# Optimization experiments

Hardware: AMD Instinct MI355X
Metric: run time of the kernel (lower is better)

The kernel has to match this reference:

```python
import jax, jax.numpy as jnp
import numpy as np

D_MODEL = 512
D_INNER = 2 * D_MODEL      # 1024
DT_RANK = D_MODEL // 16    # 32
D_STATE = 16
D_CONV = 4
NB_LAYERS = 3
BATCH = 64
SEQ = 201
CITY = 200
EPS = 1e-5


def setup_inputs() -> dict:
    key = jax.random.key(0)
    ks = jax.random.split(key, 12)
    def rn(k, shape, scale=0.02):
        return jax.random.normal(k, shape, jnp.float32) * scale
    A_init = jnp.tile(jnp.arange(1, D_STATE + 1, dtype=jnp.float32)[None, None, :],
                      (NB_LAYERS, D_INNER, 1))
    return {
        "x": jax.random.uniform(ks[0], (BATCH, SEQ, 2), jnp.float32),
        "city_count": CITY,
        "embed_W": rn(ks[1], (D_MODEL, 2), 0.5),
        "embed_b": jnp.zeros((D_MODEL,), jnp.float32),
        "norm_w": jnp.ones((NB_LAYERS, D_MODEL), jnp.float32),
        "norm_b": jnp.zeros((NB_LAYERS, D_MODEL), jnp.float32),
        "in_W": rn(ks[2], (NB_LAYERS, 2 * D_INNER, D_MODEL)),
        "conv_w": rn(ks[3], (NB_LAYERS, D_INNER, D_CONV), 0.1),
        "conv_b": jnp.zeros((NB_LAYERS, D_INNER), jnp.float32),
        "xproj_W": rn(ks[4], (NB_LAYERS, DT_RANK + 2 * D_STATE, D_INNER)),
        "dtproj_W": rn(ks[5], (NB_LAYERS, D_INNER, DT_RANK), 0.1),
        "dtproj_b": rn(ks[6], (NB_LAYERS, D_INNER), 0.5),
        "A_log": jnp.log(A_init),
        "Dskip": jnp.ones((NB_LAYERS, D_INNER), jnp.float32),
        "out_W": rn(ks[7], (NB_LAYERS, D_MODEL, D_INNER)),
        "normf_w": jnp.ones((D_MODEL,), jnp.float32),
        "normf_b": jnp.zeros((D_MODEL,), jnp.float32),
        "head_W": rn(ks[8], (CITY, D_MODEL)),
    }


def _silu(v):
    return v * jax.nn.sigmoid(v)


def _layernorm(v, w, b):
    v = v.astype(jnp.float32)
    mu = v.mean(-1, keepdims=True)
    var = ((v - mu) ** 2).mean(-1, keepdims=True)
    return (v - mu) * jax.lax.rsqrt(var + EPS) * w + b


def _rmsnorm(v, w, b):
    v = v.astype(jnp.float32)
    ms = (v * v).mean(-1, keepdims=True)
    return v * jax.lax.rsqrt(ms + EPS) * w + b


def _mamba_mixer(h, in_W, cw, cb, xp_W, dt_W, dt_b, A_log, Dv, o_W):
    B, L, _ = h.shape
    xz = jnp.einsum('bld,ed->ble', h, in_W)              # (B,L,2*di)
    xc, z = jnp.split(xz, 2, axis=-1)
    # causal depthwise conv over time
    xt = xc.transpose(0, 2, 1)                           # (B,di,L)
    xt = jax.lax.conv_general_dilated(
        xt, cw[:, None, :], (1,), [(D_CONV - 1, 0)],
        dimension_numbers=('NCH', 'OIH', 'NCH'),
        feature_group_count=D_INNER)
    u = _silu((xt + cb[None, :, None]).transpose(0, 2, 1))   # (B,L,di)
    x_dbl = jnp.einsum('bld,ed->ble', u, xp_W)
    dt_r = x_dbl[..., :DT_RANK]
    Bm = x_dbl[..., DT_RANK:DT_RANK + D_STATE]
    Cm = x_dbl[..., DT_RANK + D_STATE:]
    dt = jax.nn.softplus(jnp.einsum('blr,dr->bld', dt_r, dt_W) + dt_b)
    A = -jnp.exp(A_log)                                  # (di,n)

    def step(hst, ins):
        dt_t, B_t, C_t, u_t = ins                        # (B,di),(B,n),(B,n),(B,di)
        dA = jnp.exp(dt_t[..., None] * A)                # (B,di,n)
        hst = dA * hst + (dt_t * u_t)[..., None] * B_t[:, None, :]
        y = jnp.einsum('bdn,bn->bd', hst, C_t)
        return hst, y

    h0 = jnp.zeros((B, D_INNER, D_STATE), h.dtype)
    _, ys = jax.lax.scan(step, h0, (dt.transpose(1, 0, 2), Bm.transpose(1, 0, 2),
                                    Cm.transpose(1, 0, 2), u.transpose(1, 0, 2)))
    y = ys.transpose(1, 0, 2) + Dv * u
    y = y * _silu(z)
    return jnp.einsum('bld,ed->ble', y, o_W)


def reference(x, city_count, embed_W, embed_b, norm_w, norm_b, in_W, conv_w, conv_b,
              xproj_W, dtproj_W, dtproj_b, A_log, Dskip, out_W, normf_w, normf_b, head_W):
    h = jnp.einsum('blc,dc->bld', x, embed_W) + embed_b
    residual = None
    for i in range(NB_LAYERS):
        residual = h if residual is None else h + residual   # residual in fp32
        hn = _layernorm(residual, norm_w[i], norm_b[i])
        h = _mamba_mixer(hn, in_W[i], conv_w[i], conv_b[i], xproj_W[i],
                         dtproj_W[i], dtproj_b[i], A_log[i], Dskip[i], out_W[i])
    residual = h + residual
    xf = _rmsnorm(residual, normf_w, normf_b)                # final fused RMSNorm
    logits = jnp.einsum('bld,cd->blc', xf, head_W)           # output head -> city logits
    return logits
```

## Files before the change

### kernel.cpp

```cpp
#include <hip/hip_runtime.h>
#include <hip/hip_fp16.h>
#include <math.h>

#define D_MODEL 512
#define D_INNER 1024
#define DT_RANK 32
#define D_STATE 16
#define D_CONV 4
#define NB_LAYERS 3
#define BATCH 64
#define SEQ 201
#define CITY 200
#define M_ROWS (BATCH * SEQ)
#define M_PAD 12928
#define EPS 1e-5f
#define NCH 8
#define CL 26

typedef __attribute__((ext_vector_type(8))) short short8;
typedef __attribute__((ext_vector_type(8))) unsigned short ushort8;
typedef __attribute__((ext_vector_type(4))) float f32x4;

__device__ __forceinline__ float sigmoidf_(float x) { return 1.f / (1.f + __expf(-x)); }

__device__ __forceinline__ unsigned short f2b(float f) {
  union { float f; unsigned int u; } v; v.f = f;
  unsigned int r = (v.u + 0x7fff + ((v.u >> 16) & 1)) >> 16;
  return (unsigned short)r;
}
__device__ __forceinline__ float b2f(unsigned short h) {
  union { unsigned int u; float f; } v; v.u = ((unsigned int)h) << 16; return v.f;
}
__device__ __forceinline__ unsigned short f2h(float f) {
  __half h = __float2half(f); return *(unsigned short*)&h;
}
__device__ __forceinline__ float h2f(unsigned short u) {
  __half h = *(__half*)&u; return __half2float(h);
}

__device__ __forceinline__ void gload_lds16(const void* g, void* l) {
  __builtin_amdgcn_global_load_lds(
      (const __attribute__((address_space(1))) void*)g,
      (__attribute__((address_space(3))) void*)l, 16, 0, 0);
}

__device__ __forceinline__ void exp_vec(float dtv, const float* __restrict__ Areg,
                                        bool fast, float* __restrict__ e) {
  if (fast) {
    float e1 = __expf(-dtv);
    e[0] = e1;
    e[1] = e1 * e1;
    e[2] = e[1] * e1;
    e[3] = e[1] * e[1];
    e[4] = e[3] * e1;
    e[5] = e[3] * e[1];
    e[6] = e[3] * e[2];
    e[7] = e[3] * e[3];
    e[8] = e[7] * e1;
    e[9] = e[7] * e[1];
    e[10] = e[7] * e[2];
    e[11] = e[7] * e[3];
    e[12] = e[7] * e[4];
    e[13] = e[7] * e[5];
    e[14] = e[7] * e[6];
    e[15] = e[7] * e[7];
  } else {
#pragma unroll
    for (int n = 0; n < D_STATE; ++n) e[n] = __expf(dtv * Areg[n]);
  }
}
__device__ __forceinline__ bool a_is_arange(const float* __restrict__ Areg) {
  bool f = true;
#pragma unroll
  for (int n = 0; n < D_STATE; ++n)
    f = f && (fabsf(Areg[n] + (float)(n + 1)) < 1e-4f * (float)(n + 1));
  return f;
}

__global__ __launch_bounds__(256) void k_f2b(const float* __restrict__ in,
                                             unsigned short* __restrict__ out,
                                             int n, int n_total) {
  int i = blockIdx.x * 256 + threadIdx.x;
  if (i < n) out[i] = f2b(in[i]);
  else if (i < n_total) out[i] = 0;
}

__global__ __launch_bounds__(256) void k_padR(const float* __restrict__ W,
                                              unsigned short* __restrict__ out,
                                              int nl, int inrows, int outrows, int cols) {
  int i = blockIdx.x * 256 + threadIdx.x;
  if (i >= nl * outrows * cols) return;
  int c = i % cols;
  int r = (i / cols) % outrows;
  int L = i / (cols * outrows);
  out[i] = (r < inrows) ? f2b(W[((size_t)L * inrows + r) * cols + c]) : 0;
}

__global__ __launch_bounds__(256) void k_convT(const float* __restrict__ cw,
                                               float* __restrict__ cwT) {
  int i = blockIdx.x * 256 + threadIdx.x;
  if (i >= NB_LAYERS * D_CONV * D_INNER) return;
  int d = i & (D_INNER - 1);
  int k = (i >> 10) & 3;
  int L = i >> 12;
  cwT[i] = cw[((size_t)L * D_INNER + d) * D_CONV + k];
}

__global__ __launch_bounds__(256) void k_embed(const float* __restrict__ x,
                                               const float* __restrict__ W,
                                               const float* __restrict__ b,
                                               float* __restrict__ res) {
  int idx = blockIdx.x * 256 + threadIdx.x;
  if (idx >= M_ROWS * D_MODEL) return;
  int d = idx & (D_MODEL - 1);
  int m = idx >> 9;
  float x0 = x[m * 2 + 0], x1 = x[m * 2 + 1];
  res[idx] = fmaf(x0, W[d * 2 + 0], fmaf(x1, W[d * 2 + 1], b[d]));
}

__global__ __launch_bounds__(256) void k_norm(const float* __restrict__ res,
                                              unsigned short* __restrict__ out_b,
                                              const float* __restrict__ w,
                                              const float* __restrict__ b,
                                              int mode) {
  int row = blockIdx.x * 4 + (threadIdx.x >> 6);
  int lane = threadIdx.x & 63;
  if (row >= M_ROWS) return;
  const float* rp = res + (size_t)row * D_MODEL;
  float v[8];
#pragma unroll
  for (int j = 0; j < 8; ++j) v[j] = rp[j * 64 + lane];
  float mu = 0.f, rstd;
  if (mode == 0) {
    float s = 0.f;
#pragma unroll
    for (int j = 0; j < 8; ++j) s += v[j];
#pragma unroll
    for (int o = 1; o < 64; o <<= 1) s += __shfl_xor(s, o);
    mu = s * (1.f / D_MODEL);
    float vs = 0.f;
#pragma unroll
    for (int j = 0; j < 8; ++j) { float d0 = v[j] - mu; vs += d0 * d0; }
#pragma unroll
    for (int o = 1; o < 64; o <<= 1) vs += __shfl_xor(vs, o);
    rstd = rsqrtf(vs * (1.f / D_MODEL) + EPS);
  } else {
    float s = 0.f;
#pragma unroll
    for (int j = 0; j < 8; ++j) s += v[j] * v[j];
#pragma unroll
    for (int o = 1; o < 64; o <<= 1) s += __shfl_xor(s, o);
    rstd = rsqrtf(s * (1.f / D_MODEL) + EPS);
  }
#pragma unroll
  for (int j = 0; j < 8; ++j) {
    int c = j * 64 + lane;
    out_b[(size_t)row * D_MODEL + c] = f2b((v[j] - mu) * rstd * w[c] + b[c]);
  }
}

template <int BOUT, int ADDRES>
__global__ __launch_bounds__(256) void k_gemm_mfma(const unsigned short* __restrict__ A,
                                                   const unsigned short* __restrict__ B,
                                                   void* __restrict__ Cv, int ldc,
                                                   int M, int Nout, int K) {
  __shared__ unsigned short lA[2][128 * 64];
  __shared__ unsigned short lB[2][128 * 64];
  int tid = threadIdx.x;
  int wave = tid >> 6, lane = tid & 63;
  int nx = gridDim.x;
  int nwg = nx * gridDim.y;
  int bid = blockIdx.y * nx + blockIdx.x;
  int q = nwg >> 3, rr = nwg & 7;
  int xcd = bid & 7, idx = bid >> 3;
  int swz = (xcd < rr ? xcd * (q + 1) : rr * (q + 1) + (xcd - rr) * q) + idx;
  int bm = (swz / nx) * 128, bn = (swz % nx) * 128;
  int wm = (wave >> 1) * 64, wn = (wave & 1) * 64;
  f32x4 acc[4][4] = {};

  auto stage = [&](int kt, int bb) {
    int k0 = kt * 64;
#pragma unroll
    for (int i = 0; i < 4; ++i) {
      int e = (i * 256 + tid) * 8;
      int r = e >> 6, c = e & 63;
      int csrc = c ^ ((r & 7) << 3);
      gload_lds16(A + (size_t)(bm + r) * K + k0 + csrc, &lA[bb][e]);
      gload_lds16(B + (size_t)(bn + r) * K + k0 + csrc, &lB[bb][e]);
    }
  };

  int nk = K >> 6;
  stage(0, 0);
  __syncthreads();
  for (int t = 0; t < nk; ++t) {
    int cur = t & 1;
    if (t + 1 < nk) stage(t + 1, cur ^ 1);
#pragma unroll
    for (int ks = 0; ks < 2; ++ks) {
      int koff = ks * 32 + (lane >> 4) * 8;
      short8 a[4], b[4];
#pragma unroll
      for (int i = 0; i < 4; ++i) {
        int row = wm + i * 16 + (lane & 15);
        a[i] = *(const short8*)&lA[cur][row * 64 + (koff ^ ((row & 7) << 3))];
      }
#pragma unroll
      for (int j = 0; j < 4; ++j) {
        int row = wn + j * 16 + (lane & 15);
        b[j] = *(const short8*)&lB[cur][row * 64 + (koff ^ ((row & 7) << 3))];
      }
#pragma unroll
      for (int i = 0; i < 4; ++i)
#pragma unroll
        for (int j = 0; j < 4; ++j)
          acc[i][j] = __builtin_amdgcn_mfma_f32_16x16x32_bf16(a[i], b[j], acc[i][j], 0, 0, 0);
    }
    __syncthreads();
  }
#pragma unroll
  for (int i = 0; i < 4; ++i) {
    int row0 = bm + wm + i * 16 + (lane >> 4) * 4;
#pragma unroll
    for (int j = 0; j < 4; ++j) {
      int col = bn + wn + j * 16 + (lane & 15);
#pragma unroll
      for (int r = 0; r < 4; ++r) {
        int m = row0 + r;
        if (m < M && col < Nout) {
          float v = acc[i][j][r];
          if (ADDRES) {
            float* cp = (float*)Cv + (size_t)m * ldc + col;
            *cp = *cp + v;
          } else if (BOUT == 1) {
            ((unsigned short*)Cv)[(size_t)m * ldc + col] = f2b(v);
          } else {
            ((float*)Cv)[(size_t)m * ldc + col] = v;
          }
        }
      }
    }
  }
}

__global__ __launch_bounds__(256) void k_conv_silu(const unsigned short* __restrict__ xz,
                                                   const float* __restrict__ cwT,
                                                   const float* __restrict__ cb,
                                                   unsigned short* __restrict__ ub) {
  int i = blockIdx.x * 256 + threadIdx.x;
  if (i >= M_ROWS * 128) return;
  int dg = (i & 127) << 3;
  int m = i >> 7;
  int l = m % SEQ;
  float y[8];
  float4 cb0 = *(const float4*)&cb[dg];
  float4 cb1 = *(const float4*)&cb[dg + 4];
  y[0] = cb0.x; y[1] = cb0.y; y[2] = cb0.z; y[3] = cb0.w;
  y[4] = cb1.x; y[5] = cb1.y; y[6] = cb1.z; y[7] = cb1.w;
#pragma unroll
  for (int k = 0; k < D_CONV; ++k) {
    int ls = l - (D_CONV - 1) + k;
    if (ls >= 0) {
      ushort8 xv = *(const ushort8*)&xz[(size_t)(m - (D_CONV - 1) + k) * 2048 + dg];
      float4 w0 = *(const float4*)&cwT[k * D_INNER + dg];
      float4 w1 = *(const float4*)&cwT[k * D_INNER + dg + 4];
      y[0] = fmaf(w0.x, b2f(xv[0]), y[0]);
      y[1] = fmaf(w0.y, b2f(xv[1]), y[1]);
      y[2] = fmaf(w0.z, b2f(xv[2]), y[2]);
      y[3] = fmaf(w0.w, b2f(xv[3]), y[3]);
      y[4] = fmaf(w1.x, b2f(xv[4]), y[4]);
      y[5] = fmaf(w1.y, b2f(xv[5]), y[5]);
      y[6] = fmaf(w1.z, b2f(xv[6]), y[6]);
      y[7] = fmaf(w1.w, b2f(xv[7]), y[7]);
    }
  }
  ushort8 o;
#pragma unroll
  for (int j = 0; j < 8; ++j) { float v = y[j]; v = v * sigmoidf_(v); o[j] = f2b(v); }
  *(ushort8*)&ub[(size_t)m * D_INNER + dg] = o;
}

__device__ __forceinline__ float dt_eval(const float* __restrict__ xq,
                                         const float* __restrict__ Wd, float bias) {
  float a0 = 0.f, a1 = 0.f, a2 = 0.f, a3 = 0.f;
#pragma unroll
  for (int r = 0; r < 2; ++r) {
    float4 q0 = *(const float4*)&xq[r * 16 + 0];
    float4 q1 = *(const float4*)&xq[r * 16 + 4];
    float4 q2 = *(const float4*)&xq[r * 16 + 8];
    float4 q3 = *(const float4*)&xq[r * 16 + 12];
    int o = r * 16;
    a0 = fmaf(q0.x, Wd[o + 0], a0); a0 = fmaf(q0.y, Wd[o + 1], a0);
    a0 = fmaf(q0.z, Wd[o + 2], a0); a0 = fmaf(q0.w, Wd[o + 3], a0);
    a1 = fmaf(q1.x, Wd[o + 4], a1); a1 = fmaf(q1.y, Wd[o + 5], a1);
    a1 = fmaf(q1.z, Wd[o + 6], a1); a1 = fmaf(q1.w, Wd[o + 7], a1);
    a2 = fmaf(q2.x, Wd[o + 8], a2); a2 = fmaf(q2.y, Wd[o + 9], a2);
    a2 = fmaf(q2.z, Wd[o + 10], a2); a2 = fmaf(q2.w, Wd[o + 11], a2);
    a3 = fmaf(q3.x, Wd[o + 12], a3); a3 = fmaf(q3.y, Wd[o + 13], a3);
    a3 = fmaf(q3.z, Wd[o + 14], a3); a3 = fmaf(q3.w, Wd[o + 15], a3);
  }
  float dot = ((a0 + a1) + (a2 + a3)) + bias;
  return (dot > 20.f) ? dot : __logf(1.f + __expf(dot));
}

__global__ __launch_bounds__(256) void k_scan_p1(const unsigned short* __restrict__ ub,
                                                 const float* __restrict__ xdb,
                                                 const float* __restrict__ dtW,
                                                 const float* __restrict__ dtb,
                                                 const float* __restrict__ A_log,
                                                 unsigned short* __restrict__ dt,
                                                 unsigned short* __restrict__ L,
                                                 float* __restrict__ dtsum) {
  int tid = threadIdx.x;
  int b = blockIdx.x >> 3, c = blockIdx.x & 7;
  int d = blockIdx.y * 256 + tid;
  int t0 = c * CL, t1 = t0 + CL < SEQ ? t0 + CL : SEQ;
  float Wd[DT_RANK];
#pragma unroll
  for (int r = 0; r < DT_RANK; r += 4) {
    float4 w4 = *(const float4*)&dtW[(size_t)d * DT_RANK + r];
    Wd[r] = w4.x; Wd[r + 1] = w4.y; Wd[r + 2] = w4.z; Wd[r + 3] = w4.w;
  }
  float bias = dtb[d];
  float Areg[D_STATE], hst[D_STATE];
#pragma unroll
  for (int n = 0; n < D_STATE; ++n) {
    Areg[n] = -__expf(A_log[d * D_STATE + n]);
    hst[n] = 0.f;
  }
  bool fast = a_is_arange(Areg);
  float ds = 0.f;
  size_t row0 = (size_t)b * SEQ;
  for (int t = t0; t < t1; ++t) {
    size_t m = row0 + t;
    const float* xq = xdb + m * 64;
    unsigned short dh = f2h(dt_eval(xq, Wd, bias));
    dt[m * D_INNER + d] = dh;
    float dtv = h2f(dh);
    float uv = b2f(ub[m * D_INNER + d]);
    float Bv[D_STATE];
#pragma unroll
    for (int qd = 0; qd < 4; ++qd) {
      float4 v4 = *(const float4*)&xq[32 + qd * 4];
      Bv[qd * 4 + 0] = v4.x; Bv[qd * 4 + 1] = v4.y;
      Bv[qd * 4 + 2] = v4.z; Bv[qd * 4 + 3] = v4.w;
    }
    float du = dtv * uv;
    ds += dtv;
    float e[D_STATE];
    exp_vec(dtv, Areg, fast, e);
#pragma unroll
    for (int j = 0; j < D_STATE; ++j)
      hst[j] = fmaf(e[j], hst[j], du * Bv[j]);
  }
  size_t base = ((size_t)(b * NCH + c) * D_INNER + d) * D_STATE;
  ushort8 o0, o1;
#pragma unroll
  for (int j = 0; j < 8; ++j) { o0[j] = f2b(hst[j]); o1[j] = f2b(hst[8 + j]); }
  *(ushort8*)&L[base] = o0;
  *(ushort8*)&L[base + 8] = o1;
  dtsum[(size_t)(b * NCH + c) * D_INNER + d] = ds;
}

__global__ __launch_bounds__(256) void k_scan_fix(const float* __restrict__ A_log,
                                                  const float* __restrict__ dtsum,
                                                  unsigned short* __restrict__ L) {
  int tid = threadIdx.x;
  int b = blockIdx.x;
  int d = blockIdx.y * 256 + tid;
  float Areg[D_STATE], h[D_STATE];
#pragma unroll
  for (int n = 0; n < D_STATE; ++n) {
    Areg[n] = -__expf(A_log[d * D_STATE + n]);
    h[n] = 0.f;
  }
  bool fast = a_is_arange(Areg);
  for (int c = 0; c < NCH; ++c) {
    size_t base = ((size_t)(b * NCH + c) * D_INNER + d) * D_STATE;
    ushort8 l0 = *(const ushort8*)&L[base];
    ushort8 l1 = *(const ushort8*)&L[base + 8];
    float ds = dtsum[(size_t)(b * NCH + c) * D_INNER + d];
    ushort8 o0, o1;
#pragma unroll
    for (int j = 0; j < 8; ++j) { o0[j] = f2b(h[j]); o1[j] = f2b(h[8 + j]); }
    *(ushort8*)&L[base] = o0;
    *(ushort8*)&L[base + 8] = o1;
    float e[D_STATE];
    exp_vec(ds, Areg, fast, e);
#pragma unroll
    for (int j = 0; j < 8; ++j)
      h[j] = fmaf(e[j], h[j], b2f(l0[j]));
#pragma unroll
    for (int j = 0; j < 8; ++j)
      h[8 + j] = fmaf(e[8 + j], h[8 + j], b2f(l1[j]));
  }
}

__global__ __launch_bounds__(256) void k_scan_p2(const unsigned short* __restrict__ xz,
                                                 const unsigned short* __restrict__ ub,
                                                 const float* __restrict__ xdb,
                                                 const unsigned short* __restrict__ dt,
                                                 const float* __restrict__ A_log,
                                                 const float* __restrict__ Dv,
                                                 const unsigned short* __restrict__ L,
                                                 unsigned short* __restrict__ yb) {
  int tid = threadIdx.x;
  int b = blockIdx.x >> 3, c = blockIdx.x & 7;
  int d = blockIdx.y * 256 + tid;
  int t0 = c * CL, t1 = t0 + CL < SEQ ? t0 + CL : SEQ;
  float Areg[D_STATE], hst[D_STATE];
  size_t base = ((size_t)(b * NCH + c) * D_INNER + d) * D_STATE;
  ushort8 l0 = *(const ushort8*)&L[base];
  ushort8 l1 = *(const ushort8*)&L[base + 8];
#pragma unroll
  for (int n = 0; n < D_STATE; ++n) Areg[n] = -__expf(A_log[d * D_STATE + n]);
  bool fast = a_is_arange(Areg);
#pragma unroll
  for (int j = 0; j < 8; ++j) { hst[j] = b2f(l0[j]); hst[8 + j] = b2f(l1[j]); }
  float Dd = Dv[d];
  size_t row0 = (size_t)b * SEQ;
  for (int t = t0; t < t1; ++t) {
    size_t m = row0 + t;
    const float* xq = xdb + m * 64;
    float dtv = h2f(dt[m * D_INNER + d]);
    float uv = b2f(ub[m * D_INNER + d]);
    float zv = b2f(xz[m * 2048 + 1024 + d]);
    float Bv[D_STATE], Cvv[D_STATE];
#pragma unroll
    for (int qd = 0; qd < 4; ++qd) {
      float4 v4 = *(const float4*)&xq[32 + qd * 4];
      Bv[qd * 4 + 0] = v4.x; Bv[qd * 4 + 1] = v4.y;
      Bv[qd * 4 + 2] = v4.z; Bv[qd * 4 + 3] = v4.w;
      float4 c4 = *(const float4*)&xq[48 + qd * 4];
      Cvv[qd * 4 + 0] = c4.x; Cvv[qd * 4 + 1] = c4.y;
      Cvv[qd * 4 + 2] = c4.z; Cvv[qd * 4 + 3] = c4.w;
    }
    float du = dtv * uv;
    float e[D_STATE];
    exp_vec(dtv, Areg, fast, e);
    float y0 = 0.f, y1 = 0.f, y2 = 0.f, y3 = 0.f;
#pragma unroll
    for (int j = 0; j < D_STATE; ++j) {
      hst[j] = fmaf(e[j], hst[j], du * Bv[j]);
      float& yq = (j < 4) ? y0 : (j < 8) ? y1 : (j < 12) ? y2 : y3;
      yq = fmaf(hst[j], Cvv[j], yq);
    }
    float y = (y0 + y1) + (y2 + y3);
    y = fmaf(Dd, uv, y);
    y = y * (zv * sigmoidf_(zv));
    yb[m * D_INNER + d] = f2b(y);
  }
}

extern "C" void kernel_launch(void* const* d_in, const int* in_sizes, int n_in,
                              void* d_out, int out_size, void* d_ws, size_t ws_size,
                              hipStream_t stream) {
  const float* x        = (const float*)d_in[0];
  const float* embed_W  = (const float*)d_in[2];
  const float* embed_b  = (const float*)d_in[3];
  const float* norm_w   = (const float*)d_in[4];
  const float* norm_b   = (const float*)d_in[5];
  const float* in_W     = (const float*)d_in[6];
  const float* conv_w   = (const float*)d_in[7];
  const float* conv_b   = (const float*)d_in[8];
  const float* xproj_W  = (const float*)d_in[9];
  const float* dtproj_W = (const float*)d_in[10];
  const float* dtproj_b = (const float*)d_in[11];
  const float* A_log    = (const float*)d_in[12];
  const float* Dskip    = (const float*)d_in[13];
  const float* out_W    = (const float*)d_in[14];
  const float* normf_w  = (const float*)d_in[15];
  const float* normf_b  = (const float*)d_in[16];
  const float* head_W   = (const float*)d_in[17];
  float* out = (float*)d_out;

  size_t f32_elems = (size_t)M_ROWS * 512  + (size_t)M_PAD * 64  +
                     (size_t)NB_LAYERS * D_CONV * D_INNER  +
                     (size_t)BATCH * NCH * D_INNER ;
  size_t bf16_elems = (size_t)M_ROWS * 2048  + (size_t)M_PAD * 2048  +
                      (size_t)M_ROWS * 1024  +
                      (size_t)BATCH * NCH * D_INNER * D_STATE  +
                      (size_t)NB_LAYERS * (2048 * 512 + 512 * 1024 + 128 * 1024) +
                      256 * 512;
  size_t need = f32_elems * 4 + bf16_elems * 2;
  if (ws_size < need) return;

  float* ws = (float*)d_ws;
  float* buf_res  = ws;
  float* buf_xdb  = buf_res  + (size_t)M_ROWS * 512;
  float* buf_cwT  = buf_xdb  + (size_t)M_PAD * 64;
  float* buf_dts  = buf_cwT  + (size_t)NB_LAYERS * D_CONV * D_INNER;
  unsigned short* buf_xz   = (unsigned short*)(buf_dts + (size_t)BATCH * NCH * D_INNER);
  unsigned short* buf_ub   = buf_xz + (size_t)M_ROWS * 2048;
  unsigned short* buf_yb   = buf_ub + (size_t)M_PAD * 1024;
  unsigned short* buf_hnb  = buf_yb;
  unsigned short* buf_dt   = buf_yb + (size_t)M_PAD * 1024;
  unsigned short* buf_L    = buf_dt + (size_t)M_ROWS * 1024;
  unsigned short* buf_wib  = buf_L + (size_t)BATCH * NCH * D_INNER * D_STATE;
  unsigned short* buf_wob  = buf_wib + (size_t)NB_LAYERS * 2048 * 512;
  unsigned short* buf_wxb  = buf_wob + (size_t)NB_LAYERS * 512 * 1024;
  unsigned short* buf_whb  = buf_wxb + (size_t)NB_LAYERS * 128 * 1024;

  dim3 blk(256);

  k_f2b<<<(NB_LAYERS * 2048 * 512 + 255) / 256, blk, 0, stream>>>(
      in_W, buf_wib, NB_LAYERS * 2048 * 512, NB_LAYERS * 2048 * 512);
  k_f2b<<<(NB_LAYERS * 512 * 1024 + 255) / 256, blk, 0, stream>>>(
      out_W, buf_wob, NB_LAYERS * 512 * 1024, NB_LAYERS * 512 * 1024);
  k_padR<<<(NB_LAYERS * 128 * 1024 + 255) / 256, blk, 0, stream>>>(
      xproj_W, buf_wxb, NB_LAYERS, 64, 128, 1024);
  k_f2b<<<(256 * 512 + 255) / 256, blk, 0, stream>>>(head_W, buf_whb, CITY * 512, 256 * 512);
  k_convT<<<(NB_LAYERS * D_CONV * D_INNER + 255) / 256, blk, 0, stream>>>(conv_w, buf_cwT);

  k_embed<<<(M_ROWS * D_MODEL + 255) / 256, blk, 0, stream>>>(x, embed_W, embed_b, buf_res);

  for (int i = 0; i < NB_LAYERS; ++i) {
    k_norm<<<(M_ROWS + 3) / 4, blk, 0, stream>>>(
        buf_res, buf_hnb, norm_w + i * D_MODEL, norm_b + i * D_MODEL, 0);

    k_gemm_mfma<1, 0><<<dim3(2048 / 128, M_PAD / 128), blk, 0, stream>>>(
        buf_hnb, buf_wib + (size_t)i * 2048 * 512, buf_xz, 2048, M_ROWS, 2048, 512);

    k_conv_silu<<<(M_ROWS * 128 + 255) / 256, blk, 0, stream>>>(
        buf_xz, buf_cwT + (size_t)i * D_CONV * D_INNER, conv_b + (size_t)i * D_INNER, buf_ub);

    k_gemm_mfma<0, 0><<<dim3(1, M_PAD / 128), blk, 0, stream>>>(
        buf_ub, buf_wxb + (size_t)i * 128 * 1024, buf_xdb, 64, M_ROWS, 64, 1024);

    const float* Ai  = A_log + (size_t)i * D_INNER * D_STATE;
    const float* Wdt = dtproj_W + (size_t)i * D_INNER * DT_RANK;
    const float* bdt = dtproj_b + (size_t)i * D_INNER;
    k_scan_p1<<<dim3(BATCH * NCH, D_INNER / 256), blk, 0, stream>>>(
        buf_ub, buf_xdb, Wdt, bdt, Ai, buf_dt, buf_L, buf_dts);
    k_scan_fix<<<dim3(BATCH, D_INNER / 256), blk, 0, stream>>>(Ai, buf_dts, buf_L);
    k_scan_p2<<<dim3(BATCH * NCH, D_INNER / 256), blk, 0, stream>>>(
        buf_xz, buf_ub, buf_xdb, buf_dt, Ai, Dskip + (size_t)i * D_INNER, buf_L, buf_yb);

    k_gemm_mfma<0, 1><<<dim3(512 / 128, M_PAD / 128), blk, 0, stream>>>(
        buf_yb, buf_wob + (size_t)i * 512 * 1024, buf_res, 512, M_ROWS, 512, 1024);
  }

  k_norm<<<(M_ROWS + 3) / 4, blk, 0, stream>>>(buf_res, buf_hnb, normf_w, normf_b, 1);

  k_gemm_mfma<0, 0><<<dim3(256 / 128, M_PAD / 128), blk, 0, stream>>>(
      buf_hnb, buf_whb, out, CITY, M_ROWS, CITY, 512);
}
```

Before: 746.6 us.

## Single-buffer GEMM LDS staging and fold chunk-state fixup into scan pass 2

The GEMM drops its double-buffered LDS prefetch and uses a single buffer, with a load, sync, compute, sync loop. The separate k_scan_fix kernel is removed. Each k_scan_p2 block now recomputes its starting state by serially combining all earlier chunk states and dt sums. This saves a launch and the L rewrite, but the early chunks are recomputed redundantly, and the GEMM loses its load/compute overlap and may stall more on memory.

```diff
diff --git a/kernel.cpp b/kernel.cpp
--- a/kernel.cpp
+++ b/kernel.cpp
@@ -164,8 +164,8 @@
                                                    const unsigned short* __restrict__ B,
                                                    void* __restrict__ Cv, int ldc,
                                                    int M, int Nout, int K) {
-  __shared__ unsigned short lA[2][128 * 64];
-  __shared__ unsigned short lB[2][128 * 64];
+  __shared__ unsigned short lA[128 * 64];
+  __shared__ unsigned short lB[128 * 64];
   int tid = threadIdx.x;
   int wave = tid >> 6, lane = tid & 63;
   int nx = gridDim.x;
@@ -178,24 +178,16 @@
   int wm = (wave >> 1) * 64, wn = (wave & 1) * 64;
   f32x4 acc[4][4] = {};
 
-  auto stage = [&](int kt, int bb) {
-    int k0 = kt * 64;
+  for (int k0 = 0; k0 < K; k0 += 64) {
 #pragma unroll
     for (int i = 0; i < 4; ++i) {
       int e = (i * 256 + tid) * 8;
       int r = e >> 6, c = e & 63;
       int csrc = c ^ ((r & 7) << 3);
-      gload_lds16(A + (size_t)(bm + r) * K + k0 + csrc, &lA[bb][e]);
-      gload_lds16(B + (size_t)(bn + r) * K + k0 + csrc, &lB[bb][e]);
-    }
-  };
-
-  int nk = K >> 6;
-  stage(0, 0);
-  __syncthreads();
-  for (int t = 0; t < nk; ++t) {
-    int cur = t & 1;
-    if (t + 1 < nk) stage(t + 1, cur ^ 1);
+      gload_lds16(A + (size_t)(bm + r) * K + k0 + csrc, &lA[e]);
+      gload_lds16(B + (size_t)(bn + r) * K + k0 + csrc, &lB[e]);
+    }
+    __syncthreads();
 #pragma unroll
     for (int ks = 0; ks < 2; ++ks) {
       int koff = ks * 32 + (lane >> 4) * 8;
@@ -203,12 +195,12 @@
 #pragma unroll
       for (int i = 0; i < 4; ++i) {
         int row = wm + i * 16 + (lane & 15);
-        a[i] = *(const short8*)&lA[cur][row * 64 + (koff ^ ((row & 7) << 3))];
+        a[i] = *(const short8*)&lA[row * 64 + (koff ^ ((row & 7) << 3))];
       }
 #pragma unroll
       for (int j = 0; j < 4; ++j) {
         int row = wn + j * 16 + (lane & 15);
-        b[j] = *(const short8*)&lB[cur][row * 64 + (koff ^ ((row & 7) << 3))];
+        b[j] = *(const short8*)&lB[row * 64 + (koff ^ ((row & 7) << 3))];
       }
 #pragma unroll
       for (int i = 0; i < 4; ++i)
@@ -362,40 +354,6 @@
   dtsum[(size_t)(b * NCH + c) * D_INNER + d] = ds;
 }
 
-__global__ __launch_bounds__(256) void k_scan_fix(const float* __restrict__ A_log,
-                                                  const float* __restrict__ dtsum,
-                                                  unsigned short* __restrict__ L) {
-  int tid = threadIdx.x;
-  int b = blockIdx.x;
-  int d = blockIdx.y * 256 + tid;
-  float Areg[D_STATE], h[D_STATE];
-#pragma unroll
-  for (int n = 0; n < D_STATE; ++n) {
-    Areg[n] = -__expf(A_log[d * D_STATE + n]);
-    h[n] = 0.f;
-  }
-  bool fast = a_is_arange(Areg);
-  for (int c = 0; c < NCH; ++c) {
-    size_t base = ((size_t)(b * NCH + c) * D_INNER + d) * D_STATE;
-    ushort8 l0 = *(const ushort8*)&L[base];
-    ushort8 l1 = *(const ushort8*)&L[base + 8];
-    float ds = dtsum[(size_t)(b * NCH + c) * D_INNER + d];
-    ushort8 o0, o1;
-#pragma unroll
-    for (int j = 0; j < 8; ++j) { o0[j] = f2b(h[j]); o1[j] = f2b(h[8 + j]); }
-    *(ushort8*)&L[base] = o0;
-    *(ushort8*)&L[base + 8] = o1;
-    float e[D_STATE];
-    exp_vec(ds, Areg, fast, e);
-#pragma unroll
-    for (int j = 0; j < 8; ++j)
-      h[j] = fmaf(e[j], h[j], b2f(l0[j]));
-#pragma unroll
-    for (int j = 0; j < 8; ++j)
-      h[8 + j] = fmaf(e[8 + j], h[8 + j], b2f(l1[j]));
-  }
-}
-
 __global__ __launch_bounds__(256) void k_scan_p2(const unsigned short* __restrict__ xz,
                                                  const unsigned short* __restrict__ ub,
                                                  const float* __restrict__ xdb,
@@ -403,20 +361,31 @@
                                                  const float* __restrict__ A_log,
                                                  const float* __restrict__ Dv,
                                                  const unsigned short* __restrict__ L,
+                                                 const float* __restrict__ dtsum,
                                                  unsigned short* __restrict__ yb) {
   int tid = threadIdx.x;
   int b = blockIdx.x >> 3, c = blockIdx.x & 7;
   int d = blockIdx.y * 256 + tid;
   int t0 = c * CL, t1 = t0 + CL < SEQ ? t0 + CL : SEQ;
   float Areg[D_STATE], hst[D_STATE];
-  size_t base = ((size_t)(b * NCH + c) * D_INNER + d) * D_STATE;
-  ushort8 l0 = *(const ushort8*)&L[base];
-  ushort8 l1 = *(const ushort8*)&L[base + 8];
-#pragma unroll
-  for (int n = 0; n < D_STATE; ++n) Areg[n] = -__expf(A_log[d * D_STATE + n]);
+#pragma unroll
+  for (int n = 0; n < D_STATE; ++n) {
+    Areg[n] = -__expf(A_log[d * D_STATE + n]);
+    hst[n] = 0.f;
+  }
   bool fast = a_is_arange(Areg);
-#pragma unroll
-  for (int j = 0; j < 8; ++j) { hst[j] = b2f(l0[j]); hst[8 + j] = b2f(l1[j]); }
+  for (int j = 0; j < c; ++j) {
+    size_t jb = ((size_t)(b * NCH + j) * D_INNER + d) * D_STATE;
+    ushort8 l0 = *(const ushort8*)&L[jb];
+    ushort8 l1 = *(const ushort8*)&L[jb + 8];
+    float ds = dtsum[(size_t)(b * NCH + j) * D_INNER + d];
+    float e[D_STATE];
+    exp_vec(ds, Areg, fast, e);
+#pragma unroll
+    for (int n = 0; n < 8; ++n) hst[n] = fmaf(e[n], hst[n], b2f(l0[n]));
+#pragma unroll
+    for (int n = 0; n < 8; ++n) hst[8 + n] = fmaf(e[8 + n], hst[8 + n], b2f(l1[n]));
+  }
   float Dd = Dv[d];
   size_t row0 = (size_t)b * SEQ;
   for (int t = t0; t < t1; ++t) {
@@ -532,9 +501,9 @@
     const float* bdt = dtproj_b + (size_t)i * D_INNER;
     k_scan_p1<<<dim3(BATCH * NCH, D_INNER / 256), blk, 0, stream>>>(
         buf_ub, buf_xdb, Wdt, bdt, Ai, buf_dt, buf_L, buf_dts);
-    k_scan_fix<<<dim3(BATCH, D_INNER / 256), blk, 0, stream>>>(Ai, buf_dts, buf_L);
     k_scan_p2<<<dim3(BATCH * NCH, D_INNER / 256), blk, 0, stream>>>(
-        buf_xz, buf_ub, buf_xdb, buf_dt, Ai, Dskip + (size_t)i * D_INNER, buf_L, buf_yb);
+        buf_xz, buf_ub, buf_xdb, buf_dt, Ai, Dskip + (size_t)i * D_INNER, buf_L, buf_dts,
+        buf_yb);
 
     k_gemm_mfma<0, 1><<<dim3(512 / 128, M_PAD / 128), blk, 0, stream>>>(
         buf_yb, buf_wob + (size_t)i * 512 * 1024, buf_res, 512, M_ROWS, 512, 1024);
```

New measurement: 752.8 us. Within noise of the previous version (+0.8%).
